# Optimization experiments

Measured on AMD Instinct MI355X. Metric: run time of the kernel, lower is better.

## Reference

```python
import jax, jax.numpy as jnp
import numpy as np

N_NODES = 50000
N_EDGES = 1600000
IN_DIM = 128
HID = 64
H1 = 2          # heads layer 0
H2 = 1          # heads layer 1
N_CLS = 16
NEG_SLOPE = 0.2


def setup_inputs() -> dict:
    key = jax.random.key(0)
    ks = jax.random.split(key, 10)
    h = jax.random.normal(ks[0], (N_NODES, IN_DIM), dtype=jnp.float32)
    src = jax.random.randint(ks[1], (N_EDGES,), 0, N_NODES, dtype=jnp.int64)
    dst = jax.random.randint(ks[2], (N_EDGES,), 0, N_NODES, dtype=jnp.int64)
    s = 0.05
    W1_src = jax.random.normal(ks[3], (IN_DIM, H1 * HID), dtype=jnp.float32) * s
    W1_dst = jax.random.normal(ks[4], (IN_DIM, H1 * HID), dtype=jnp.float32) * s
    a1 = jax.random.normal(ks[5], (H1, HID), dtype=jnp.float32) * s
    W2_src = jax.random.normal(ks[6], (H1 * HID, H2 * N_CLS), dtype=jnp.float32) * s
    W2_dst = jax.random.normal(ks[7], (H1 * HID, H2 * N_CLS), dtype=jnp.float32) * s
    a2 = jax.random.normal(ks[8], (H2, N_CLS), dtype=jnp.float32) * s
    W_res = jax.random.normal(ks[9], (H1 * HID, H2 * N_CLS), dtype=jnp.float32) * s
    return {"h": h, "src": src, "dst": dst, "W1_src": W1_src, "W1_dst": W1_dst,
            "a1": a1, "W2_src": W2_src, "W2_dst": W2_dst, "a2": a2, "W_res": W_res}


def _gatv2_conv(h, src, dst, W_src, W_dst, attn, n_nodes):
    # GATv2: e_ij = a . LeakyReLU(W_src h_j + W_dst h_i), softmax over in-edges of i
    heads, out_dim = attn.shape
    fs = (h @ W_src).reshape(-1, heads, out_dim)  # [N,H,D]
    fd = (h @ W_dst).reshape(-1, heads, out_dim)
    e = jax.nn.leaky_relu(fs[src] + fd[dst], negative_slope=NEG_SLOPE)  # [E,H,D]
    score = jnp.einsum('ehd,hd->eh', e, attn)                           # [E,H]
    m = jax.ops.segment_max(score, dst, num_segments=n_nodes)           # [N,H]
    ex = jnp.exp(score - m[dst])
    denom = jax.ops.segment_sum(ex, dst, num_segments=n_nodes)          # [N,H]
    alpha = ex / denom[dst]                                             # [E,H]
    msg = alpha[:, :, None] * fs[src]                                   # [E,H,D]
    return jax.ops.segment_sum(msg, dst, num_segments=n_nodes)          # [N,H,D]


def reference(h, src, dst, W1_src, W1_dst, a1, W2_src, W2_dst, a2, W_res):
    n = h.shape[0]
    # layer 0: GATv2Conv -> elu activation -> flatten heads
    h1 = _gatv2_conv(h, src, dst, W1_src, W1_dst, a1, n)   # [N,H1,HID]
    h1 = jax.nn.elu(h1).reshape(n, -1)                      # [N,H1*HID]
    # layer 1: GATv2Conv with residual, no activation, mean over heads
    h2 = _gatv2_conv(h1, src, dst, W2_src, W2_dst, a2, n)   # [N,H2,N_CLS]
    res = (h1 @ W_res).reshape(n, H2, N_CLS)
    logits = (h2 + res).mean(axis=1)                        # [N,N_CLS]
    return logits
```

## Files before the change

kernel.cpp:

```cpp
#include <hip/hip_runtime.h>
#include <hip/hip_bf16.h>

#define NEG 0.2f
#define FNEG_MAX -3.402823466e38f

__device__ __forceinline__ unsigned short f2bf(float f){
  unsigned u = __float_as_uint(f);
  return (unsigned short)((u + 0x7fffu + ((u >> 16) & 1u)) >> 16);
}
__device__ __forceinline__ unsigned pk2bf(float a, float b){
  return (unsigned)f2bf(a) | ((unsigned)f2bf(b) << 16);
}
__device__ __forceinline__ float bflo(unsigned u){ return __uint_as_float(u << 16); }
__device__ __forceinline__ float bfhi(unsigned u){ return __uint_as_float(u & 0xffff0000u); }

__global__ __launch_bounds__(256)
void k_count(const int* __restrict__ dst, int* __restrict__ deg,
             int* __restrict__ pos, int ne){
  int e = blockIdx.x*256 + threadIdx.x;
  if (e < ne) pos[e] = atomicAdd(&deg[dst[e]], 1);
}

#define SCB 512
__global__ __launch_bounds__(SCB)
void k_scan1(const int* __restrict__ deg, int* __restrict__ off,
             int* __restrict__ bsum, int n){
  __shared__ int lds[SCB];
  int t = threadIdx.x, i = blockIdx.x*SCB + t;
  int x = (i < n) ? deg[i] : 0;
  lds[t] = x; __syncthreads();
  for (int s = 1; s < SCB; s <<= 1){
    int v = (t >= s) ? lds[t-s] : 0;
    __syncthreads();
    lds[t] += v;
    __syncthreads();
  }
  if (i < n) off[i] = lds[t] - x;
  if (t == SCB-1) bsum[blockIdx.x] = lds[t];
}

__global__ void k_scan2(int* __restrict__ bsum, int nblk){
  if (threadIdx.x == 0 && blockIdx.x == 0){
    int acc = 0;
    for (int b = 0; b < nblk; ++b){ int v = bsum[b]; bsum[b] = acc; acc += v; }
  }
}

__global__ __launch_bounds__(SCB)
void k_scan3(int* __restrict__ off, const int* __restrict__ bsum, int n, int ne){
  int i = blockIdx.x*SCB + threadIdx.x;
  if (i < n) off[i] += bsum[blockIdx.x];
  if (i == 0) off[n] = ne;
}

__global__ __launch_bounds__(256)
void k_scatter(const int* __restrict__ src, const int* __restrict__ dst,
               const int* __restrict__ off, const int* __restrict__ pos,
               int* __restrict__ csr_src, int ne){
  int e = blockIdx.x*256 + threadIdx.x;
  if (e >= ne) return;
  int d = dst[e];
  csr_src[off[d] + pos[e]] = src[e];
}

#define GM1 32
__global__ __launch_bounds__(256)
void k_gemm1(const float* __restrict__ h, const float* __restrict__ Ws,
             const float* __restrict__ Wd, unsigned* __restrict__ fs,
             float* __restrict__ fd, int n){
  __shared__ float ht[128][36];
  int tid = threadIdx.x;
  int node0 = blockIdx.x * GM1;
  for (int i = tid; i < GM1*128; i += 256){
    int r = i >> 7, c = i & 127;
    int nd = node0 + r;
    ht[c][r] = (nd < n) ? h[(size_t)nd*128 + c] : 0.f;
  }
  __syncthreads();
  int cg  = tid & 31;
  int mat = (tid >> 5) & 1;
  int q   = tid >> 6;
  const float4* W4 = (const float4*)(mat ? Wd : Ws);
  float acc[8][4];
  #pragma unroll
  for (int j = 0; j < 8; ++j){ acc[j][0]=0.f; acc[j][1]=0.f; acc[j][2]=0.f; acc[j][3]=0.f; }
  for (int k = 0; k < 128; ++k){
    float4 w = W4[k*32 + cg];
    const float4* hp4 = (const float4*)&ht[k][q*8];
    float4 ha = hp4[0], hb = hp4[1];
    float hv[8] = {ha.x, ha.y, ha.z, ha.w, hb.x, hb.y, hb.z, hb.w};
    #pragma unroll
    for (int j = 0; j < 8; ++j){
      acc[j][0] = fmaf(hv[j], w.x, acc[j][0]);
      acc[j][1] = fmaf(hv[j], w.y, acc[j][1]);
      acc[j][2] = fmaf(hv[j], w.z, acc[j][2]);
      acc[j][3] = fmaf(hv[j], w.w, acc[j][3]);
    }
  }
  #pragma unroll
  for (int j = 0; j < 8; ++j){
    int nd = node0 + q*8 + j;
    if (nd < n){
      if (mat == 0){
        uint2 o; o.x = pk2bf(acc[j][0], acc[j][1]); o.y = pk2bf(acc[j][2], acc[j][3]);
        ((uint2*)fs)[(size_t)nd*32 + cg] = o;
      } else {
        float4 o; o.x=acc[j][0]; o.y=acc[j][1]; o.z=acc[j][2]; o.w=acc[j][3];
        ((float4*)fd)[(size_t)nd*32 + cg] = o;
      }
    }
  }
}

#define THR1 10.f
__global__ __launch_bounds__(256)
void k_l1_node(const unsigned* __restrict__ fs, const float* fdv_,
               const int* __restrict__ off, const int* __restrict__ csr,
               const float* __restrict__ a1, float* out, int n){
  int wid  = (int)((blockIdx.x*256u + threadIdx.x) >> 6);
  int lane = threadIdx.x & 63;
  if (wid >= n) return;
  int d  = wid;
  int hh = lane >> 5;
  int lp = lane & 31;
  int e0 = off[d], e1 = off[d+1];
  int deg = e1 - e0;
  const uint2* fs2v = (const uint2*)fs;
  float4 fdv = ((const float4*)fdv_)[(size_t)d*32 + lp];
  float4 aw  = ((const float4*)a1)[lp];
  float m = FNEG_MAX, den = 0.f;
  float4 acc = make_float4(0.f, 0.f, 0.f, 0.f);

  int nt = (deg + 3) & ~3;
  for (int k = 0; k < nt; k += 4){
    int eiA = e0 + k + hh;
    int eiB = eiA + 2;
    bool vA = eiA < e1, vB = eiB < e1;
    int sA = csr[vA ? eiA : e0];
    int sB = csr[vB ? eiB : e0];
    uint2 uA = fs2v[(size_t)sA*32 + lp];
    uint2 uB = fs2v[(size_t)sB*32 + lp];
    float xA0 = bflo(uA.x), xA1 = bfhi(uA.x), xA2 = bflo(uA.y), xA3 = bfhi(uA.y);
    float xB0 = bflo(uB.x), xB1 = bfhi(uB.x), xB2 = bflo(uB.y), xB3 = bfhi(uB.y);
    float pA, pB;
    {
      float t0 = xA0 + fdv.x, t1 = xA1 + fdv.y;
      float t2 = xA2 + fdv.z, t3 = xA3 + fdv.w;
      t0 = fmaxf(t0, NEG*t0); t1 = fmaxf(t1, NEG*t1);
      t2 = fmaxf(t2, NEG*t2); t3 = fmaxf(t3, NEG*t3);
      pA = fmaf(t0, aw.x, fmaf(t1, aw.y, fmaf(t2, aw.z, t3*aw.w)));
    }
    {
      float t0 = xB0 + fdv.x, t1 = xB1 + fdv.y;
      float t2 = xB2 + fdv.z, t3 = xB3 + fdv.w;
      t0 = fmaxf(t0, NEG*t0); t1 = fmaxf(t1, NEG*t1);
      t2 = fmaxf(t2, NEG*t2); t3 = fmaxf(t3, NEG*t3);
      pB = fmaf(t0, aw.x, fmaf(t1, aw.y, fmaf(t2, aw.z, t3*aw.w)));
    }
    #pragma unroll
    for (int o = 8; o >= 1; o >>= 1){
      pA += __shfl_xor(pA, o, 64);
      pB += __shfl_xor(pB, o, 64);
    }
    pA = vA ? pA : FNEG_MAX;
    pB = vB ? pB : FNEG_MAX;
    float pmax = fmaxf(pA, pB);
    if (__any(pmax > m + THR1)){
      float nm = fmaxf(m, pmax);
      float sc = __expf(m - nm);
      den *= sc;
      acc.x *= sc; acc.y *= sc; acc.z *= sc; acc.w *= sc;
      m = nm;
    }
    float wA = vA ? __expf(pA - m) : 0.f;
    float wB = vB ? __expf(pB - m) : 0.f;
    den += wA + wB;
    acc.x = fmaf(wA, xA0, fmaf(wB, xB0, acc.x));
    acc.y = fmaf(wA, xA1, fmaf(wB, xB1, acc.y));
    acc.z = fmaf(wA, xA2, fmaf(wB, xB2, acc.z));
    acc.w = fmaf(wA, xA3, fmaf(wB, xB3, acc.w));
  }

  float om   = __shfl_xor(m,   32, 64);
  float oden = __shfl_xor(den, 32, 64);
  float4 oacc;
  oacc.x = __shfl_xor(acc.x, 32, 64);
  oacc.y = __shfl_xor(acc.y, 32, 64);
  oacc.z = __shfl_xor(acc.z, 32, 64);
  oacc.w = __shfl_xor(acc.w, 32, 64);
  float nm = fmaxf(m, om);
  float s1 = __expf(m - nm), s2 = __expf(om - nm);
  den = den*s1 + oden*s2;
  float4 r;
  r.x = acc.x*s1 + oacc.x*s2;
  r.y = acc.y*s1 + oacc.y*s2;
  r.z = acc.z*s1 + oacc.z*s2;
  r.w = acc.w*s1 + oacc.w*s2;
  float inv = (den > 0.f) ? 1.f/den : 0.f;
  r.x *= inv; r.y *= inv; r.z *= inv; r.w *= inv;
  r.x = r.x > 0.f ? r.x : __expf(r.x) - 1.f;
  r.y = r.y > 0.f ? r.y : __expf(r.y) - 1.f;
  r.z = r.z > 0.f ? r.z : __expf(r.z) - 1.f;
  r.w = r.w > 0.f ? r.w : __expf(r.w) - 1.f;
  if (hh == 0) ((float4*)out)[(size_t)d*32 + lp] = r;
}

__global__ __launch_bounds__(256)
void k_gemm2(const float* __restrict__ h1, const float* __restrict__ Ws,
             const float* __restrict__ Wd, const float* __restrict__ Wr,
             unsigned short* __restrict__ fs2, float* __restrict__ fd2,
             float* __restrict__ res, int n){
  __shared__ float hs[16][129];
  __shared__ float w[3][128][16];
  int tid = threadIdx.x;
  for (int i = tid; i < 2048; i += 256){
    int k = i >> 4, j = i & 15;
    w[0][k][j] = Ws[i]; w[1][k][j] = Wd[i]; w[2][k][j] = Wr[i];
  }
  int node0 = blockIdx.x * 16;
  for (int i = tid; i < 2048; i += 256){
    int r = i >> 7, c = i & 127;
    int nd = node0 + r;
    hs[r][c] = (nd < n) ? h1[(size_t)nd*128 + c] : 0.f;
  }
  __syncthreads();
  int j = tid & 15, ni = tid >> 4;
  float as = 0.f, ad = 0.f, ar = 0.f;
  for (int k = 0; k < 128; ++k){
    float hv = hs[ni][k];
    as = fmaf(hv, w[0][k][j], as);
    ad = fmaf(hv, w[1][k][j], ad);
    ar = fmaf(hv, w[2][k][j], ar);
  }
  int nd = node0 + ni;
  if (nd < n){
    fs2[(size_t)nd*16 + j] = f2bf(as);
    fd2[(size_t)nd*16 + j] = ad;
    res[(size_t)nd*16 + j] = ar;
  }
}

#define THR2 10.f
__global__ __launch_bounds__(256)
void k_l2_node(const unsigned short* __restrict__ fs2, const float* __restrict__ fd2,
               const float* __restrict__ resd, const int* __restrict__ off,
               const int* __restrict__ csr, const float* __restrict__ a2,
               float* __restrict__ outp, int n){
  int wid  = (int)((blockIdx.x*256u + threadIdx.x) >> 6);
  int lane = threadIdx.x & 63;
  if (wid >= n) return;
  int d = wid;
  int g = lane >> 4, j = lane & 15;
  int e0 = off[d], e1 = off[d+1];
  int deg = e1 - e0;
  float fdv = fd2[(size_t)d*16 + j];
  float aw  = a2[j];
  float m = FNEG_MAX, den = 0.f, acc = 0.f;
  int jmax = (deg + 7) >> 3;
  for (int it = 0; it < jmax; ++it){
    int iA = e0 + it*8 + g;
    int iB = iA + 4;
    bool vA = iA < e1, vB = iB < e1;
    int sA = csr[vA ? iA : e0];
    int sB = csr[vB ? iB : e0];
    float xA = __uint_as_float((unsigned)fs2[(size_t)sA*16 + j] << 16);
    float xB = __uint_as_float((unsigned)fs2[(size_t)sB*16 + j] << 16);
    float tA = xA + fdv; tA = fmaxf(tA, NEG*tA);
    float tB = xB + fdv; tB = fmaxf(tB, NEG*tB);
    float pA = tA * aw, pB = tB * aw;
    #pragma unroll
    for (int o = 8; o >= 1; o >>= 1){
      pA += __shfl_xor(pA, o, 64);
      pB += __shfl_xor(pB, o, 64);
    }
    pA = vA ? pA : FNEG_MAX;
    pB = vB ? pB : FNEG_MAX;
    float pmax = fmaxf(pA, pB);
    if (__any(pmax > m + THR2)){
      float nm = fmaxf(m, pmax);
      float sc = __expf(m - nm);
      den *= sc; acc *= sc;
      m = nm;
    }
    float wA = vA ? __expf(pA - m) : 0.f;
    float wB = vB ? __expf(pB - m) : 0.f;
    den += wA + wB;
    acc = fmaf(wA, xA, fmaf(wB, xB, acc));
  }
  #pragma unroll
  for (int o = 16; o <= 32; o <<= 1){
    float om   = __shfl_xor(m,   o, 64);
    float oden = __shfl_xor(den, o, 64);
    float oacc = __shfl_xor(acc, o, 64);
    float nm = fmaxf(m, om);
    float s1 = __expf(m - nm);
    float s2 = __expf(om - nm);
    den = den*s1 + oden*s2;
    acc = acc*s1 + oacc*s2;
    m = nm;
  }
  if (g == 0){
    float inv = (den > 0.f) ? 1.f/den : 0.f;
    outp[(size_t)d*16 + j] = acc*inv + resd[(size_t)d*16 + j];
  }
}

extern "C" void kernel_launch(void* const* d_in, const int* in_sizes, int n_in,
                              void* d_out, int out_size, void* d_ws, size_t ws_size,
                              hipStream_t stream) {
  const float* h    = (const float*)d_in[0];
  const int*   src  = (const int*)  d_in[1];
  const int*   dst  = (const int*)  d_in[2];
  const float* W1s  = (const float*)d_in[3];
  const float* W1d  = (const float*)d_in[4];
  const float* a1   = (const float*)d_in[5];
  const float* W2s  = (const float*)d_in[6];
  const float* W2d  = (const float*)d_in[7];
  const float* a2   = (const float*)d_in[8];
  const float* Wres = (const float*)d_in[9];
  float* out = (float*)d_out;

  const int n  = in_sizes[0] / 128;
  const int ne = in_sizes[1];

  float* ws  = (float*)d_ws;
  float* fs1 = ws;
  float* fd1 = fs1 + (size_t)n*128;
  float* fs2 = fd1 + (size_t)n*128;
  float* fd2 = fs2 + (size_t)n*16;
  float* res = fd2 + (size_t)n*16;
  int* deg     = (int*)(res + (size_t)n*16);
  int* off     = deg + n;
  int* pos     = off + (n+1);
  int* bsum    = pos + ne;
  int* csr_src = bsum + 128;

  const int nblk = (n + SCB - 1) / SCB;

  hipMemsetAsync(deg, 0, (size_t)n*4, stream);
  k_count  <<<(ne + 255)/256, 256, 0, stream>>>(dst, deg, pos, ne);
  k_scan1  <<<nblk, SCB, 0, stream>>>(deg, off, bsum, n);
  k_scan2  <<<1, 64, 0, stream>>>(bsum, nblk);
  k_scan3  <<<nblk, SCB, 0, stream>>>(off, bsum, n, ne);
  k_scatter<<<(ne + 255)/256, 256, 0, stream>>>(src, dst, off, pos, csr_src, ne);

  k_gemm1  <<<(n + GM1 - 1)/GM1, 256, 0, stream>>>(h, W1s, W1d, (unsigned*)fs1, fd1, n);
  k_l1_node<<<(n + 3)/4, 256, 0, stream>>>((const unsigned*)fs1, fd1, off, csr_src, a1, fd1, n);

  k_gemm2  <<<(n + 15)/16, 256, 0, stream>>>(fd1, W2s, W2d, Wres, (unsigned short*)fs2, fd2, res, n);
  k_l2_node<<<(n + 3)/4, 256, 0, stream>>>((const unsigned short*)fs2, fd2, res, off, csr_src, a2, out, n);
}
```

Baseline: 316.3 us.

## Use bf16 MFMA for layer-1 projection GEMM

Replaces the scalar-FMA layer-1 GEMM with a matrix-core kernel. Each block converts a 64-node tile of h and the whole 128x128 weight matrix to bf16 in LDS, then issues 16x16x32 bf16 MFMAs. The grid gains a second dimension that separates the src and dst projections. This trades fp32 input precision for matrix-core throughput, and each block reloads and converts the full weight matrix while writing outputs as scattered scalar stores.

```diff
diff --git a/kernel.cpp b/kernel.cpp
--- a/kernel.cpp
+++ b/kernel.cpp
@@ -7,9 +7,6 @@
 __device__ __forceinline__ unsigned short f2bf(float f){
   unsigned u = __float_as_uint(f);
   return (unsigned short)((u + 0x7fffu + ((u >> 16) & 1u)) >> 16);
-}
-__device__ __forceinline__ unsigned pk2bf(float a, float b){
-  return (unsigned)f2bf(a) | ((unsigned)f2bf(b) << 16);
 }
 __device__ __forceinline__ float bflo(unsigned u){ return __uint_as_float(u << 16); }
 __device__ __forceinline__ float bfhi(unsigned u){ return __uint_as_float(u & 0xffff0000u); }
@@ -63,50 +60,53 @@
   csr_src[off[d] + pos[e]] = src[e];
 }
 
-#define GM1 32
-__global__ __launch_bounds__(256)
-void k_gemm1(const float* __restrict__ h, const float* __restrict__ Ws,
-             const float* __restrict__ Wd, unsigned* __restrict__ fs,
-             float* __restrict__ fd, int n){
-  __shared__ float ht[128][36];
+typedef __attribute__((ext_vector_type(8))) short bf16x8;
+typedef __attribute__((ext_vector_type(4))) float f32x4;
+
+__global__ __launch_bounds__(256)
+void k_gemm1m(const float* __restrict__ h, const float* __restrict__ Ws,
+              const float* __restrict__ Wd, unsigned short* __restrict__ fs,
+              float* __restrict__ fd, int n){
+  __shared__ unsigned short hs[64][144];
+  __shared__ unsigned short wsl[128][144];
   int tid = threadIdx.x;
-  int node0 = blockIdx.x * GM1;
-  for (int i = tid; i < GM1*128; i += 256){
+  int node0 = blockIdx.x * 64;
+  int mat = blockIdx.y;
+  const float* W = mat ? Wd : Ws;
+  for (int i = tid; i < 64*128; i += 256){
     int r = i >> 7, c = i & 127;
     int nd = node0 + r;
-    ht[c][r] = (nd < n) ? h[(size_t)nd*128 + c] : 0.f;
+    hs[r][c] = f2bf((nd < n) ? h[(size_t)nd*128 + c] : 0.f);
+  }
+  for (int i = tid; i < 128*128; i += 256){
+    int k = i >> 7, c = i & 127;
+    wsl[c][k] = f2bf(W[i]);
   }
   __syncthreads();
-  int cg  = tid & 31;
-  int mat = (tid >> 5) & 1;
-  int q   = tid >> 6;
-  const float4* W4 = (const float4*)(mat ? Wd : Ws);
-  float acc[8][4];
+  int w = tid >> 6, lane = tid & 63;
+  int rsel = lane & 15, ksel = (lane >> 4) * 8;
+  f32x4 acc[8];
   #pragma unroll
-  for (int j = 0; j < 8; ++j){ acc[j][0]=0.f; acc[j][1]=0.f; acc[j][2]=0.f; acc[j][3]=0.f; }
-  for (int k = 0; k < 128; ++k){
-    float4 w = W4[k*32 + cg];
-    const float4* hp4 = (const float4*)&ht[k][q*8];
-    float4 ha = hp4[0], hb = hp4[1];
-    float hv[8] = {ha.x, ha.y, ha.z, ha.w, hb.x, hb.y, hb.z, hb.w};
+  for (int cf = 0; cf < 8; ++cf){ acc[cf][0]=0.f; acc[cf][1]=0.f; acc[cf][2]=0.f; acc[cf][3]=0.f; }
+  #pragma unroll
+  for (int ks = 0; ks < 4; ++ks){
+    bf16x8 a = *(const bf16x8*)&hs[w*16 + rsel][ks*32 + ksel];
     #pragma unroll
-    for (int j = 0; j < 8; ++j){
-      acc[j][0] = fmaf(hv[j], w.x, acc[j][0]);
-      acc[j][1] = fmaf(hv[j], w.y, acc[j][1]);
-      acc[j][2] = fmaf(hv[j], w.z, acc[j][2]);
-      acc[j][3] = fmaf(hv[j], w.w, acc[j][3]);
-    }
-  }
+    for (int cf = 0; cf < 8; ++cf){
+      bf16x8 b = *(const bf16x8*)&wsl[cf*16 + rsel][ks*32 + ksel];
+      acc[cf] = __builtin_amdgcn_mfma_f32_16x16x32_bf16(a, b, acc[cf], 0, 0, 0);
+    }
+  }
+  int rq = lane >> 4;
   #pragma unroll
-  for (int j = 0; j < 8; ++j){
-    int nd = node0 + q*8 + j;
-    if (nd < n){
-      if (mat == 0){
-        uint2 o; o.x = pk2bf(acc[j][0], acc[j][1]); o.y = pk2bf(acc[j][2], acc[j][3]);
-        ((uint2*)fs)[(size_t)nd*32 + cg] = o;
-      } else {
-        float4 o; o.x=acc[j][0]; o.y=acc[j][1]; o.z=acc[j][2]; o.w=acc[j][3];
-        ((float4*)fd)[(size_t)nd*32 + cg] = o;
+  for (int cf = 0; cf < 8; ++cf){
+    #pragma unroll
+    for (int j = 0; j < 4; ++j){
+      int nd = node0 + w*16 + rq*4 + j;
+      int col = cf*16 + rsel;
+      if (nd < n){
+        if (mat == 0) fs[(size_t)nd*128 + col] = f2bf(acc[cf][j]);
+        else          fd[(size_t)nd*128 + col] = acc[cf][j];
       }
     }
   }
@@ -344,7 +344,8 @@
   k_scan3  <<<nblk, SCB, 0, stream>>>(off, bsum, n, ne);
   k_scatter<<<(ne + 255)/256, 256, 0, stream>>>(src, dst, off, pos, csr_src, ne);
 
-  k_gemm1  <<<(n + GM1 - 1)/GM1, 256, 0, stream>>>(h, W1s, W1d, (unsigned*)fs1, fd1, n);
+  k_gemm1m <<<dim3((n + 63)/64, 2), 256, 0, stream>>>(
+      h, W1s, W1d, (unsigned short*)fs1, fd1, n);
   k_l1_node<<<(n + 3)/4, 256, 0, stream>>>((const unsigned*)fs1, fd1, off, csr_src, a1, fd1, n);
 
   k_gemm2  <<<(n + 15)/16, 256, 0, stream>>>(fd1, W2s, W2d, Wres, (unsigned short*)fs2, fd2, res, n);
```

Measured after the change: 322.5 us. No clear change (+2.0%).
